# Optimization experiments

Hardware: AMD Instinct MI355X
Metric: run time of the kernel (lower is better)

Reference implementation:

```python
import jax, jax.numpy as jnp
import numpy as np

E = 512
H = 8
D = E // H
HID = 2048
NE = 4
TOPK = 2
EPS = 1e-5
NEG = -1e9


def _ln(x, w, b):
    mu = jnp.mean(x, axis=-1, keepdims=True)
    var = jnp.mean(jnp.square(x - mu), axis=-1, keepdims=True)
    return (x - mu) * jax.lax.rsqrt(var + EPS) * w + b


def _expert(xf, mask, ln1_w, ln1_b, ipw, ipb, opw, opb, ln2_w, ln2_b, w1, b1, w2, b2):
    # xf: [T, E]; mask: [T] bool (allowed keys = routed tokens)
    T = xf.shape[0]
    h = _ln(xf, ln1_w, ln1_b)
    qkv = h @ ipw.T + ipb                       # [T, 3E]
    q, k, v = jnp.split(qkv, 3, axis=-1)
    q = q.reshape(T, H, D).transpose(1, 0, 2)   # [H, T, D]
    k = k.reshape(T, H, D).transpose(1, 0, 2)
    v = v.reshape(T, H, D).transpose(1, 0, 2)
    scores = jnp.einsum('htd,hsd->hts', q, k) / jnp.sqrt(jnp.asarray(D, xf.dtype))
    scores = jnp.where(mask[None, None, :], scores, NEG)
    a = jax.nn.softmax(scores, axis=-1)
    o = jnp.einsum('hts,hsd->htd', a, v).transpose(1, 0, 2).reshape(T, E)
    o = o @ opw.T + opb
    x1 = xf + o                                 # residual (dropout = identity, eval)
    h2 = _ln(x1, ln2_w, ln2_b)
    m = jax.nn.gelu(h2 @ w1.T + b1, approximate=False) @ w2.T + b2
    return x1 + m


def setup_inputs() -> dict:
    key = jax.random.key(0)
    ks = jax.random.split(key, 16)
    s = 0.02
    inp = {
        'x': jax.random.normal(ks[0], (4, 512, E), dtype=jnp.float32),
        'gate_w': jax.random.normal(ks[1], (NE, E), dtype=jnp.float32) * s,
        'gate_b': jnp.zeros((NE,), jnp.float32),
        'ln1_w': jnp.ones((NE, E), jnp.float32),
        'ln1_b': jnp.zeros((NE, E), jnp.float32),
        'in_proj_w': jax.random.normal(ks[2], (NE, 3 * E, E), dtype=jnp.float32) * s,
        'in_proj_b': jnp.zeros((NE, 3 * E), jnp.float32),
        'out_proj_w': jax.random.normal(ks[3], (NE, E, E), dtype=jnp.float32) * s,
        'out_proj_b': jnp.zeros((NE, E), jnp.float32),
        'ln2_w': jnp.ones((NE, E), jnp.float32),
        'ln2_b': jnp.zeros((NE, E), jnp.float32),
        'mlp_w1': jax.random.normal(ks[4], (NE, HID, E), dtype=jnp.float32) * s,
        'mlp_b1': jnp.zeros((NE, HID), jnp.float32),
        'mlp_w2': jax.random.normal(ks[5], (NE, E, HID), dtype=jnp.float32) * s,
        'mlp_b2': jnp.zeros((NE, E), jnp.float32),
    }
    return inp


def reference(x, gate_w, gate_b, ln1_w, ln1_b, in_proj_w, in_proj_b, out_proj_w,
              out_proj_b, ln2_w, ln2_b, mlp_w1, mlp_b1, mlp_w2, mlp_b2):
    B, N, _ = x.shape
    T = B * N
    xf = x.reshape(T, E)
    logits = xf @ gate_w.T + gate_b                      # [T, NE]
    topk_val, topk_idx = jax.lax.top_k(logits, TOPK)
    probs = jax.nn.softmax(topk_val, axis=-1)            # [T, TOPK]
    out = jnp.zeros_like(xf)
    for kk in range(TOPK):
        idx = topk_idx[:, kk]
        w = probs[:, kk][:, None]
        for e in range(NE):
            mask = idx == e
            eo = _expert(xf, mask,
                         ln1_w[e], ln1_b[e], in_proj_w[e], in_proj_b[e],
                         out_proj_w[e], out_proj_b[e], ln2_w[e], ln2_b[e],
                         mlp_w1[e], mlp_b1[e], mlp_w2[e], mlp_b2[e])
            out = out + jnp.where(mask[:, None], eo * w, 0.0)
    return out.reshape(B, N, E)
```

## Files before the change

### kernel.cpp

```cpp
#include <hip/hip_runtime.h>
#include <hip/hip_bf16.h>

#define T_TOK 2048
#define E_DIM 512
#define NHEAD 8
#define DHEAD 64
#define HID_D 2048
#define NEXP 4
#define NROW_ (2 * T_TOK)
#define VT_STRIDE 4352

typedef short short8 __attribute__((ext_vector_type(8)));
typedef float floatx4 __attribute__((ext_vector_type(4)));

__device__ __forceinline__ void gld16(const void* g, void* l) {
  __builtin_amdgcn_global_load_lds((const __attribute__((address_space(1))) void*)g,
                                   (__attribute__((address_space(3))) void*)l, 16, 0, 0);
}

__device__ inline float wave_sum(float v) {
  for (int off = 32; off > 0; off >>= 1) v += __shfl_xor(v, off);
  return v;
}

__device__ __forceinline__ unsigned pack_bf2(float a, float b) {
  __hip_bfloat16 ha = __float2bfloat16(a), hb = __float2bfloat16(b);
  unsigned ua = *(unsigned short*)&ha, ub = *(unsigned short*)&hb;
  return ua | (ub << 16);
}

__device__ __forceinline__ void cvt4(const float* __restrict__ s, __hip_bfloat16* __restrict__ d,
                                     int i4, int n) {
  if (i4 < n) {
    float4 v = *reinterpret_cast<const float4*>(s + i4);
    __hip_bfloat16 tmp[4] = {__float2bfloat16(v.x), __float2bfloat16(v.y),
                             __float2bfloat16(v.z), __float2bfloat16(v.w)};
    *reinterpret_cast<ushort4*>(d + i4) = *reinterpret_cast<const ushort4*>(tmp);
  }
}

__global__ void cvt_weights(const float* __restrict__ s0, const float* __restrict__ s1,
                            const float* __restrict__ s2, const float* __restrict__ s3,
                            __hip_bfloat16* d0, __hip_bfloat16* d1,
                            __hip_bfloat16* d2, __hip_bfloat16* d3,
                            int n0, int n1, int n2, int n3) {
  int i4 = (blockIdx.x * 256 + threadIdx.x) * 4;
  cvt4(s0, d0, i4, n0);
  cvt4(s1, d1, i4, n1);
  cvt4(s2, d2, i4, n2);
  cvt4(s3, d3, i4, n3);
}

__global__ void gate_kernel(const float* __restrict__ x, const float* __restrict__ gw,
                            const float* __restrict__ gb, int* token_e, float* token_p) {
  int wid = threadIdx.x >> 6, lane = threadIdx.x & 63;
  int t = blockIdx.x * 4 + wid;
  float a0 = 0, a1 = 0, a2 = 0, a3 = 0;
  for (int i = 0; i < 8; i++) {
    int c = lane + 64 * i;
    float xv = x[(size_t)t * E_DIM + c];
    a0 += xv * gw[0 * E_DIM + c];
    a1 += xv * gw[1 * E_DIM + c];
    a2 += xv * gw[2 * E_DIM + c];
    a3 += xv * gw[3 * E_DIM + c];
  }
  a0 = wave_sum(a0); a1 = wave_sum(a1); a2 = wave_sum(a2); a3 = wave_sum(a3);
  if (lane == 0) {
    float lg[4] = {a0 + gb[0], a1 + gb[1], a2 + gb[2], a3 + gb[3]};
    int i0 = 0;
    for (int e = 1; e < 4; e++) if (lg[e] > lg[i0]) i0 = e;
    int i1 = -1;
    for (int e = 0; e < 4; e++) {
      if (e == i0) continue;
      if (i1 < 0 || lg[e] > lg[i1]) i1 = e;
    }
    float e1 = __expf(lg[i1] - lg[i0]);
    float inv = 1.f / (1.f + e1);
    token_e[t] = i0; token_e[T_TOK + t] = i1;
    token_p[t] = inv; token_p[T_TOK + t] = e1 * inv;
  }
}

__global__ void count_kernel(const int* __restrict__ token_e, int* counts) {
  int g = blockIdx.x, kk = g >> 2, e = g & 3;
  __shared__ int ws4[4];
  int tid = threadIdx.x, wid = tid >> 6, lane = tid & 63;
  int c = 0;
  for (int t = tid; t < T_TOK; t += 256) c += (token_e[kk * T_TOK + t] == e);
  for (int off = 32; off; off >>= 1) c += __shfl_xor(c, off);
  if (lane == 0) ws4[wid] = c;
  __syncthreads();
  if (tid == 0) counts[g] = ws4[0] + ws4[1] + ws4[2] + ws4[3];
}

__global__ void offs_kernel(const int* __restrict__ counts, int* offs, int* padoffs) {
  int o = 0, po = 0;
  offs[0] = 0; padoffs[0] = 0;
  for (int g = 0; g < 8; g++) {
    o += counts[g]; offs[g + 1] = o;
    po += (counts[g] + 31) & ~31; padoffs[g + 1] = po;
  }
}

__global__ void compact_kernel(const int* __restrict__ token_e, const int* __restrict__ offs,
                               const int* __restrict__ padoffs, int* perm, int* rowg,
                               int* pmap, int* invrow) {
  int g = blockIdx.x, kk = g >> 2, e = g & 3;
  __shared__ int wcnt[4];
  __shared__ int base;
  int tid = threadIdx.x, wid = tid >> 6, lane = tid & 63;
  int og = offs[g], pg = padoffs[g];
  if (tid == 0) base = 0;
  __syncthreads();
  for (int t0 = 0; t0 < T_TOK; t0 += 256) {
    int t = t0 + tid;
    bool pred = token_e[kk * T_TOK + t] == e;
    unsigned long long mask = __ballot(pred);
    int rank = __popcll(mask & ((1ull << lane) - 1ull));
    if (lane == 0) wcnt[wid] = __popcll(mask);
    __syncthreads();
    int woff = 0;
    for (int i = 0; i < wid; i++) woff += wcnt[i];
    if (pred) {
      int row = og + base + woff + rank;
      perm[row] = t;
      rowg[row] = g;
      pmap[row] = pg + (row - og);
      invrow[kk * T_TOK + t] = row;
    }
    __syncthreads();
    if (tid == 0) base += wcnt[0] + wcnt[1] + wcnt[2] + wcnt[3];
    __syncthreads();
  }
}

__global__ void ln_kernel(const float* __restrict__ src, const int* __restrict__ perm,
                          const int* __restrict__ rowg, const float* __restrict__ lnw,
                          const float* __restrict__ lnb, __hip_bfloat16* __restrict__ dst) {
  int wid = threadIdx.x >> 6, lane = threadIdx.x & 63;
  int row = blockIdx.x * 4 + wid;
  int e = rowg[row] & 3;
  const float* xr = src + (size_t)(perm ? perm[row] : row) * E_DIM;
  float v[8];
  float s = 0;
  for (int i = 0; i < 8; i++) { v[i] = xr[lane + 64 * i]; s += v[i]; }
  s = wave_sum(s);
  float mu = s * (1.f / 512.f);
  float q = 0;
  for (int i = 0; i < 8; i++) { float d = v[i] - mu; q += d * d; }
  q = wave_sum(q);
  float rstd = rsqrtf(q * (1.f / 512.f) + 1e-5f);
  for (int i = 0; i < 8; i++) {
    int c = lane + 64 * i;
    dst[(size_t)row * E_DIM + c] =
        __float2bfloat16((v[i] - mu) * rstd * lnw[e * E_DIM + c] + lnb[e * E_DIM + c]);
  }
}

__global__ void transpose_v(const short* __restrict__ v, const int* __restrict__ pmap,
                            short* __restrict__ vT) {
  __shared__ short tile[64][65];
  int r0 = blockIdx.x * 64, c0 = blockIdx.y * 64;
  int tc = threadIdx.x & 63, tr4 = threadIdx.x >> 6;
  for (int i = 0; i < 64; i += 4)
    tile[tr4 + i][tc] = v[(size_t)(r0 + tr4 + i) * E_DIM + c0 + tc];
  __syncthreads();
  int pcol = pmap[r0 + tc];
  for (int i = 0; i < 64; i += 4)
    vT[(size_t)(c0 + tr4 + i) * VT_STRIDE + pcol] = tile[tc][tr4 + i];
}

__global__ void zero_gaps(const int* __restrict__ offs, const int* __restrict__ padoffs,
                          short* __restrict__ vT) {
  int g = blockIdx.x;
  int cnt = offs[g + 1] - offs[g];
  int gap = (padoffs[g + 1] - padoffs[g]) - cnt;
  if ((int)threadIdx.x < gap) {
    int col = padoffs[g] + cnt + threadIdx.x;
    for (int d = blockIdx.y; d < E_DIM; d += gridDim.y)
      vT[(size_t)d * VT_STRIDE + col] = 0;
  }
}

__global__ __launch_bounds__(256) void attn_mfma(
    const short* __restrict__ qb, const short* __restrict__ kb,
    const short* __restrict__ vT, const int* __restrict__ offs,
    const int* __restrict__ padoffs, __hip_bfloat16* __restrict__ ob) {
  int d0 = blockIdx.x;
  int g = d0 & 7;
  int rem = d0 >> 3;
  int h = rem >> 5;
  int qblk = rem & 31;
  int sbeg = offs[g], rend = offs[g + 1];
  int q0 = sbeg + qblk * 64;
  if (q0 >= rend) return;
  int G = rend - sbeg;
  int pg = padoffs[g];
  int tid = threadIdx.x, wid = tid >> 6, lane = tid & 63;
  int fr = lane & 15, lg = lane >> 4;
  int qw = q0 + wid * 16;

  __shared__ short Kt[2][32 * 64];
  __shared__ short Vt[2][64 * 32];

  int arow = qw + fr; if (arow > rend - 1) arow = rend - 1;
  const short* qp = qb + (size_t)arow * E_DIM + h * DHEAD;
  short8 qf0 = *reinterpret_cast<const short8*>(qp + lg * 8);
  short8 qf1 = *reinterpret_cast<const short8*>(qp + 32 + lg * 8);

  int offB = tid * 16;
  int krow = offB >> 7, kinner = offB & 127;
  int ksrc = (kinner ^ ((krow & 7) << 4)) >> 1;
  int vd = offB >> 6, vinner = offB & 63;
  int vsrc = (vinner ^ ((vd & 3) << 4)) >> 1;
  int wb = wid * 512;
  const short* vrow = vT + (size_t)(h * DHEAD + vd) * VT_STRIDE + pg;

  auto stage = [&](int buf, int kbase) {
    int gr = sbeg + kbase + krow; if (gr > NROW_ - 1) gr = NROW_ - 1;
    gld16(kb + (size_t)gr * E_DIM + h * DHEAD + ksrc, &Kt[buf][wb]);
    gld16(vrow + kbase + vsrc, &Vt[buf][wb]);
  };

  floatx4 acc[4] = {};
  float m_r = -1e30f, l_r = 0.f;

  stage(0, 0);
  asm volatile("s_waitcnt vmcnt(0)" ::: "memory");
  __syncthreads();

  int cur = 0;
  for (int kbase = 0; kbase < G; kbase += 32) {
    if (kbase + 32 < G) stage(cur ^ 1, kbase + 32);
    const char* Kb = (const char*)&Kt[cur][0];
    const char* Vb = (const char*)&Vt[cur][0];

    int r0r = fr, r1r = 16 + fr;
    short8 kf00 = *reinterpret_cast<const short8*>(Kb + r0r * 128 + ((lg * 16) ^ ((r0r & 7) << 4)));
    short8 kf01 = *reinterpret_cast<const short8*>(Kb + r0r * 128 + ((64 + lg * 16) ^ ((r0r & 7) << 4)));
    short8 kf10 = *reinterpret_cast<const short8*>(Kb + r1r * 128 + ((lg * 16) ^ ((r1r & 7) << 4)));
    short8 kf11 = *reinterpret_cast<const short8*>(Kb + r1r * 128 + ((64 + lg * 16) ^ ((r1r & 7) << 4)));

    floatx4 s0 = {}, s1 = {};
    s0 = __builtin_amdgcn_mfma_f32_16x16x32_bf16(kf00, qf0, s0, 0, 0, 0);
    s0 = __builtin_amdgcn_mfma_f32_16x16x32_bf16(kf01, qf1, s0, 0, 0, 0);
    s1 = __builtin_amdgcn_mfma_f32_16x16x32_bf16(kf10, qf0, s1, 0, 0, 0);
    s1 = __builtin_amdgcn_mfma_f32_16x16x32_bf16(kf11, qf1, s1, 0, 0, 0);

    float sv[8];
    float mloc = -1e30f;
#pragma unroll
    for (int j = 0; j < 4; j++) {
      int k0 = kbase + lg * 4 + j;
      sv[j] = (k0 < G) ? s0[j] * 0.125f : -1e30f;
      sv[4 + j] = (k0 + 16 < G) ? s1[j] * 0.125f : -1e30f;
      mloc = fmaxf(mloc, fmaxf(sv[j], sv[4 + j]));
    }
    mloc = fmaxf(mloc, __shfl_xor(mloc, 16));
    mloc = fmaxf(mloc, __shfl_xor(mloc, 32));
    float mn = fmaxf(m_r, mloc);
    float corr = __expf(m_r - mn);
    m_r = mn;
    float p[8], sl = 0.f;
#pragma unroll
    for (int i = 0; i < 8; i++) { p[i] = __expf(sv[i] - mn); sl += p[i]; }
    sl += __shfl_xor(sl, 16);
    sl += __shfl_xor(sl, 32);
    l_r = l_r * corr + sl;

    unsigned pk0 = pack_bf2(p[0], p[1]), pk1 = pack_bf2(p[2], p[3]);
    unsigned pk2 = pack_bf2(p[4], p[5]), pk3 = pack_bf2(p[6], p[7]);
    int sA = fr + 16 * (2 * (lg & 1));
    int sB = sA + 16;
    unsigned a0 = __shfl(pk0, sA), a2 = __shfl(pk2, sA);
    unsigned b0 = __shfl(pk1, sA), b2 = __shfl(pk3, sA);
    unsigned c0 = __shfl(pk0, sB), c2 = __shfl(pk2, sB);
    unsigned d0v = __shfl(pk1, sB), d2 = __shfl(pk3, sB);
    bool hi = lg >= 2;
    union { unsigned u[4]; short8 s8; } pfu;
    pfu.u[0] = hi ? a2 : a0; pfu.u[1] = hi ? b2 : b0;
    pfu.u[2] = hi ? c2 : c0; pfu.u[3] = hi ? d2 : d0v;

    float cq[4];
#pragma unroll
    for (int j = 0; j < 4; j++) cq[j] = __shfl(corr, lg * 4 + j);
#pragma unroll
    for (int db = 0; db < 4; db++)
#pragma unroll
      for (int j = 0; j < 4; j++) acc[db][j] *= cq[j];

#pragma unroll
    for (int db = 0; db < 4; db++) {
      int dd = db * 16 + fr;
      short8 vf = *reinterpret_cast<const short8*>(Vb + dd * 64 + ((lg * 16) ^ ((dd & 3) << 4)));
      acc[db] = __builtin_amdgcn_mfma_f32_16x16x32_bf16(pfu.s8, vf, acc[db], 0, 0, 0);
    }

    asm volatile("s_waitcnt vmcnt(0)" ::: "memory");
    __syncthreads();
    cur ^= 1;
  }

  float lq[4];
#pragma unroll
  for (int j = 0; j < 4; j++) lq[j] = __shfl(l_r, lg * 4 + j);
#pragma unroll
  for (int db = 0; db < 4; db++)
#pragma unroll
    for (int j = 0; j < 4; j++) {
      int row = qw + lg * 4 + j;
      if (row < rend)
        ob[(size_t)row * E_DIM + h * DHEAD + db * 16 + fr] = __float2bfloat16(acc[db][j] / lq[j]);
    }
}

template <int MODE>
__global__ __launch_bounds__(256) void gemm_mfma(
    const short* __restrict__ A, const short* __restrict__ Wb,
    const float* __restrict__ bias, const int* __restrict__ offs,
    const int* __restrict__ perm, const float* __restrict__ resid,
    __hip_bfloat16* __restrict__ bq, __hip_bfloat16* __restrict__ bk,
    __hip_bfloat16* __restrict__ bv, float* __restrict__ outf) {
  constexpr int K = (MODE == 3) ? HID_D : E_DIM;
  constexpr int N = (MODE == 0) ? 3 * E_DIM : (MODE == 2) ? HID_D : E_DIM;
  constexpr int NKSTEP = K / 64;
  constexpr int NXB = 32;
  __shared__ short Abuf[2][4096];
  __shared__ short Bbuf[2][4096];

  int d = blockIdx.x;
  int g = d & 7;
  int rem = d >> 3;
  int yb = rem / NXB, xb = rem % NXB;
  int e = g & 3;
  int rbeg = offs[g], rend = offs[g + 1];
  int row0 = rbeg + xb * 64;
  if (row0 >= rend) return;
  int col0 = yb * 64;
  int tid = threadIdx.x;
  int wid = tid >> 6, lane = tid & 63;
  int wm = wid >> 1, wn = wid & 1;
  int fr = lane & 15, lg = lane >> 4;
  const short* wbase = Wb + (size_t)e * N * K;

  int st_row[2], st_src[2], st_arow[2];
  int wavebase = wid << 9;
  for (int c = 0; c < 2; c++) {
    int off = c * 4096 + tid * 16;
    int trow = off >> 7;
    int inner = off & 127;
    st_row[c] = trow;
    st_src[c] = (inner ^ ((trow & 7) << 4)) >> 1;
    int ga = row0 + trow;
    st_arow[c] = ga < rend ? ga : rend - 1;
  }

  auto stage = [&](int buf, int kb) {
#pragma unroll
    for (int c = 0; c < 2; c++) {
      gld16(A + (size_t)st_arow[c] * K + kb + st_src[c], &Abuf[buf][c * 2048 + wavebase]);
      gld16(wbase + (size_t)(col0 + st_row[c]) * K + kb + st_src[c],
            &Bbuf[buf][c * 2048 + wavebase]);
    }
  };

  floatx4 acc[2][2] = {};
  stage(0, 0);
  asm volatile("s_waitcnt vmcnt(0)" ::: "memory");
  __syncthreads();

  int cur = 0;
  for (int t = 0; t < NKSTEP; ++t) {
    if (t + 1 < NKSTEP) stage(cur ^ 1, (t + 1) * 64);
    const char* Ab = (const char*)&Abuf[cur][0];
    const char* Bb = (const char*)&Bbuf[cur][0];
    short8 af[2][2], bf8[2][2];
#pragma unroll
    for (int mi = 0; mi < 2; mi++)
#pragma unroll
      for (int ks = 0; ks < 2; ks++) {
        int row = wm * 32 + mi * 16 + fr;
        int cb = ks * 64 + lg * 16;
        af[mi][ks] = *reinterpret_cast<const short8*>(Ab + row * 128 + (cb ^ ((row & 7) << 4)));
      }
#pragma unroll
    for (int ni = 0; ni < 2; ni++)
#pragma unroll
      for (int ks = 0; ks < 2; ks++) {
        int row = wn * 32 + ni * 16 + fr;
        int cb = ks * 64 + lg * 16;
        bf8[ni][ks] = *reinterpret_cast<const short8*>(Bb + row * 128 + (cb ^ ((row & 7) << 4)));
      }
#pragma unroll
    for (int mi = 0; mi < 2; mi++)
#pragma unroll
      for (int ni = 0; ni < 2; ni++) {
        acc[mi][ni] = __builtin_amdgcn_mfma_f32_16x16x32_bf16(af[mi][0], bf8[ni][0], acc[mi][ni], 0, 0, 0);
        acc[mi][ni] = __builtin_amdgcn_mfma_f32_16x16x32_bf16(af[mi][1], bf8[ni][1], acc[mi][ni], 0, 0, 0);
      }
    asm volatile("s_waitcnt vmcnt(0)" ::: "memory");
    __syncthreads();
    cur ^= 1;
  }

  for (int mi = 0; mi < 2; mi++)
    for (int ni = 0; ni < 2; ni++)
      for (int j = 0; j < 4; j++) {
        int row = row0 + wm * 32 + mi * 16 + lg * 4 + j;
        if (row >= rend) continue;
        int col = col0 + wn * 32 + ni * 16 + fr;
        float val = acc[mi][ni][j] + bias[e * N + col];
        if constexpr (MODE == 0) {
          if (col < E_DIM) bq[(size_t)row * E_DIM + col] = __float2bfloat16(val);
          else if (col < 2 * E_DIM) bk[(size_t)row * E_DIM + col - E_DIM] = __float2bfloat16(val);
          else bv[(size_t)row * E_DIM + col - 2 * E_DIM] = __float2bfloat16(val);
        } else if constexpr (MODE == 1) {
          int t = perm[row];
          outf[(size_t)row * E_DIM + col] = val + resid[(size_t)t * E_DIM + col];
        } else if constexpr (MODE == 2) {
          float gl = 0.5f * val * (1.f + erff(val * 0.70710678118654752f));
          bq[(size_t)row * HID_D + col] = __float2bfloat16(gl);
        } else {
          outf[(size_t)row * E_DIM + col] = val + resid[(size_t)row * E_DIM + col];
        }
      }
}

__global__ void combine_kernel(const float* __restrict__ y, const int* __restrict__ invrow,
                               const float* __restrict__ token_p, float* __restrict__ out) {
  int t = blockIdx.x;
  int r0 = invrow[t], r1 = invrow[T_TOK + t];
  float p0 = token_p[t], p1 = token_p[T_TOK + t];
  const float* y0 = y + (size_t)r0 * E_DIM;
  const float* y1 = y + (size_t)r1 * E_DIM;
  float* o = out + (size_t)t * E_DIM;
  for (int i = threadIdx.x; i < E_DIM; i += 256) o[i] = p0 * y0[i] + p1 * y1[i];
}

extern "C" void kernel_launch(void* const* d_in, const int* in_sizes, int n_in,
                              void* d_out, int out_size, void* d_ws, size_t ws_size,
                              hipStream_t stream) {
  const float* x      = (const float*)d_in[0];
  const float* gate_w = (const float*)d_in[1];
  const float* gate_b = (const float*)d_in[2];
  const float* ln1_w  = (const float*)d_in[3];
  const float* ln1_b  = (const float*)d_in[4];
  const float* ipw    = (const float*)d_in[5];
  const float* ipb    = (const float*)d_in[6];
  const float* opw    = (const float*)d_in[7];
  const float* opb    = (const float*)d_in[8];
  const float* ln2_w  = (const float*)d_in[9];
  const float* ln2_b  = (const float*)d_in[10];
  const float* w1     = (const float*)d_in[11];
  const float* b1     = (const float*)d_in[12];
  const float* w2     = (const float*)d_in[13];
  const float* b2     = (const float*)d_in[14];
  float* out = (float*)d_out;

  const int SZ_IP = NEXP * 3 * E_DIM * E_DIM;
  const int SZ_OP = NEXP * E_DIM * E_DIM;
  const int SZ_W1 = NEXP * HID_D * E_DIM;
  const int SZ_W2 = NEXP * E_DIM * HID_D;
  const int NROW = NROW_;

  char* ws = (char*)d_ws;
  size_t off = 0;
  auto carve = [&](size_t bytes) -> void* {
    void* p = ws + off;
    off += (bytes + 255) & ~(size_t)255;
    return p;
  };
  __hip_bfloat16* ipw_bf = (__hip_bfloat16*)carve((size_t)SZ_IP * 2);
  __hip_bfloat16* opw_bf = (__hip_bfloat16*)carve((size_t)SZ_OP * 2);
  __hip_bfloat16* w1_bf  = (__hip_bfloat16*)carve((size_t)SZ_W1 * 2);
  __hip_bfloat16* w2_bf  = (__hip_bfloat16*)carve((size_t)SZ_W2 * 2);
  __hip_bfloat16* h_bf   = (__hip_bfloat16*)carve((size_t)NROW * E_DIM * 2);
  __hip_bfloat16* q_bf   = (__hip_bfloat16*)carve((size_t)NROW * E_DIM * 2);
  __hip_bfloat16* k_bf   = (__hip_bfloat16*)carve((size_t)NROW * E_DIM * 2);
  __hip_bfloat16* v_bf   = (__hip_bfloat16*)carve((size_t)NROW * E_DIM * 2);
  __hip_bfloat16* o_bf   = (__hip_bfloat16*)carve((size_t)NROW * E_DIM * 2);
  __hip_bfloat16* h2_bf  = (__hip_bfloat16*)carve((size_t)NROW * E_DIM * 2);
  __hip_bfloat16* mid_bf = (__hip_bfloat16*)carve((size_t)NROW * HID_D * 2);
  short* vT     = (short*)carve((size_t)E_DIM * VT_STRIDE * 2);
  float* x1     = (float*)carve((size_t)NROW * E_DIM * 4);
  int* token_e  = (int*)carve((size_t)NROW * 4);
  float* token_p= (float*)carve((size_t)NROW * 4);
  int* perm     = (int*)carve((size_t)NROW * 4);
  int* rowg     = (int*)carve((size_t)NROW * 4);
  int* pmap     = (int*)carve((size_t)NROW * 4);
  int* invrow   = (int*)carve((size_t)NROW * 4);
  int* counts   = (int*)carve(8 * 4);
  int* offs     = (int*)carve(9 * 4);
  int* padoffs  = (int*)carve(9 * 4);
  float* ybuf = (float*)h_bf;

  cvt_weights<<<SZ_W1 / 4 / 256, 256, 0, stream>>>(ipw, opw, w1, w2, ipw_bf, opw_bf,
                                                   w1_bf, w2_bf, SZ_IP, SZ_OP, SZ_W1, SZ_W2);
  gate_kernel<<<T_TOK / 4, 256, 0, stream>>>(x, gate_w, gate_b, token_e, token_p);
  count_kernel<<<8, 256, 0, stream>>>(token_e, counts);
  offs_kernel<<<1, 1, 0, stream>>>(counts, offs, padoffs);
  compact_kernel<<<8, 256, 0, stream>>>(token_e, offs, padoffs, perm, rowg, pmap, invrow);
  ln_kernel<<<NROW / 4, 256, 0, stream>>>(x, perm, rowg, ln1_w, ln1_b, h_bf);
  gemm_mfma<0><<<8 * 24 * 32, 256, 0, stream>>>((const short*)h_bf, (const short*)ipw_bf,
      ipb, offs, perm, nullptr, q_bf, k_bf, v_bf, nullptr);
  transpose_v<<<dim3(NROW / 64, E_DIM / 64), 256, 0, stream>>>((const short*)v_bf, pmap, vT);
  zero_gaps<<<dim3(8, 64), 32, 0, stream>>>(offs, padoffs, vT);
  attn_mfma<<<8 * 8 * 32, 256, 0, stream>>>((const short*)q_bf, (const short*)k_bf,
      vT, offs, padoffs, o_bf);
  gemm_mfma<1><<<8 * 8 * 32, 256, 0, stream>>>((const short*)o_bf, (const short*)opw_bf,
      opb, offs, perm, x, nullptr, nullptr, nullptr, x1);
  ln_kernel<<<NROW / 4, 256, 0, stream>>>(x1, nullptr, rowg, ln2_w, ln2_b, h2_bf);
  gemm_mfma<2><<<8 * 32 * 32, 256, 0, stream>>>((const short*)h2_bf, (const short*)w1_bf,
      b1, offs, perm, nullptr, mid_bf, nullptr, nullptr, nullptr);
  gemm_mfma<3><<<8 * 8 * 32, 256, 0, stream>>>((const short*)mid_bf, (const short*)w2_bf,
      b2, offs, perm, x1, nullptr, nullptr, nullptr, ybuf);
  combine_kernel<<<T_TOK, 256, 0, stream>>>(ybuf, invrow, token_p, out);
  (void)in_sizes; (void)n_in; (void)ws_size;
}
```

Baseline: 194.0 us.

## Skip softmax rescale below threshold and drop P shuffles in attention PV

In the attention kernel, the online-softmax correction (exp, shuffles and rescaling of the accumulators) now runs only when some lane's running max rises by more than a threshold. This is the lazy-rescale trick: it is exact in the end because the normalizer is rescaled consistently, but it relies on the unscaled exponentials staying bounded. The P-to-A-operand cross-lane shuffles are removed. Instead, the kernel issues two half-zeroed MFMAs per output block that read V with a new LDS swizzle matching the score layout, which doubles the PV MFMA count in exchange for fewer shuffles.

```diff
diff --git a/kernel.cpp b/kernel.cpp
--- a/kernel.cpp
+++ b/kernel.cpp
@@ -211,15 +211,15 @@
   int offB = tid * 16;
   int krow = offB >> 7, kinner = offB & 127;
   int ksrc = (kinner ^ ((krow & 7) << 4)) >> 1;
-  int vd = offB >> 6, vinner = offB & 63;
-  int vsrc = (vinner ^ ((vd & 3) << 4)) >> 1;
+  int vL = offB ^ (((offB >> 7) & 7) << 4);
+  int vd = vL >> 6, vkey0 = (vL & 63) >> 1;
   int wb = wid * 512;
   const short* vrow = vT + (size_t)(h * DHEAD + vd) * VT_STRIDE + pg;
 
   auto stage = [&](int buf, int kbase) {
     int gr = sbeg + kbase + krow; if (gr > NROW_ - 1) gr = NROW_ - 1;
     gld16(kb + (size_t)gr * E_DIM + h * DHEAD + ksrc, &Kt[buf][wb]);
-    gld16(vrow + kbase + vsrc, &Vt[buf][wb]);
+    gld16(vrow + kbase + vkey0, &Vt[buf][wb]);
   };
 
   floatx4 acc[4] = {};
@@ -258,42 +258,42 @@
     }
     mloc = fmaxf(mloc, __shfl_xor(mloc, 16));
     mloc = fmaxf(mloc, __shfl_xor(mloc, 32));
-    float mn = fmaxf(m_r, mloc);
-    float corr = __expf(m_r - mn);
-    m_r = mn;
+    if (__any(mloc > m_r + 8.f)) {
+      float mn = fmaxf(m_r, mloc);
+      float corr = __expf(m_r - mn);
+      m_r = mn;
+      l_r *= corr;
+      float cq0 = __shfl(corr, lg * 4 + 0), cq1 = __shfl(corr, lg * 4 + 1);
+      float cq2 = __shfl(corr, lg * 4 + 2), cq3 = __shfl(corr, lg * 4 + 3);
+#pragma unroll
+      for (int db = 0; db < 4; db++) {
+        acc[db][0] *= cq0; acc[db][1] *= cq1; acc[db][2] *= cq2; acc[db][3] *= cq3;
+      }
+    }
     float p[8], sl = 0.f;
 #pragma unroll
-    for (int i = 0; i < 8; i++) { p[i] = __expf(sv[i] - mn); sl += p[i]; }
+    for (int i = 0; i < 8; i++) { p[i] = __expf(sv[i] - m_r); sl += p[i]; }
     sl += __shfl_xor(sl, 16);
     sl += __shfl_xor(sl, 32);
-    l_r = l_r * corr + sl;
-
-    unsigned pk0 = pack_bf2(p[0], p[1]), pk1 = pack_bf2(p[2], p[3]);
-    unsigned pk2 = pack_bf2(p[4], p[5]), pk3 = pack_bf2(p[6], p[7]);
-    int sA = fr + 16 * (2 * (lg & 1));
-    int sB = sA + 16;
-    unsigned a0 = __shfl(pk0, sA), a2 = __shfl(pk2, sA);
-    unsigned b0 = __shfl(pk1, sA), b2 = __shfl(pk3, sA);
-    unsigned c0 = __shfl(pk0, sB), c2 = __shfl(pk2, sB);
-    unsigned d0v = __shfl(pk1, sB), d2 = __shfl(pk3, sB);
-    bool hi = lg >= 2;
-    union { unsigned u[4]; short8 s8; } pfu;
-    pfu.u[0] = hi ? a2 : a0; pfu.u[1] = hi ? b2 : b0;
-    pfu.u[2] = hi ? c2 : c0; pfu.u[3] = hi ? d2 : d0v;
-
-    float cq[4];
-#pragma unroll
-    for (int j = 0; j < 4; j++) cq[j] = __shfl(corr, lg * 4 + j);
-#pragma unroll
-    for (int db = 0; db < 4; db++)
-#pragma unroll
-      for (int j = 0; j < 4; j++) acc[db][j] *= cq[j];
+    l_r += sl;
+
+    union { unsigned u[4]; short8 s8; } pa0, pa1;
+    pa0.u[0] = pack_bf2(p[0], p[1]); pa0.u[1] = pack_bf2(p[2], p[3]);
+    pa0.u[2] = 0; pa0.u[3] = 0;
+    pa1.u[0] = pack_bf2(p[4], p[5]); pa1.u[1] = pack_bf2(p[6], p[7]);
+    pa1.u[2] = 0; pa1.u[3] = 0;
 
 #pragma unroll
     for (int db = 0; db < 4; db++) {
       int dd = db * 16 + fr;
-      short8 vf = *reinterpret_cast<const short8*>(Vb + dd * 64 + ((lg * 16) ^ ((dd & 3) << 4)));
-      acc[db] = __builtin_amdgcn_mfma_f32_16x16x32_bf16(pfu.s8, vf, acc[db], 0, 0, 0);
+      int s = ((dd >> 1) & 7) << 4;
+      uint2 w0 = *reinterpret_cast<const uint2*>(Vb + ((dd * 64 + lg * 8) ^ s));
+      uint2 w1 = *reinterpret_cast<const uint2*>(Vb + ((dd * 64 + 32 + lg * 8) ^ s));
+      union { unsigned u[4]; short8 s8; } bv0, bv1;
+      bv0.u[0] = w0.x; bv0.u[1] = w0.y; bv0.u[2] = 0; bv0.u[3] = 0;
+      bv1.u[0] = w1.x; bv1.u[1] = w1.y; bv1.u[2] = 0; bv1.u[3] = 0;
+      acc[db] = __builtin_amdgcn_mfma_f32_16x16x32_bf16(pa0.s8, bv0.s8, acc[db], 0, 0, 0);
+      acc[db] = __builtin_amdgcn_mfma_f32_16x16x32_bf16(pa1.s8, bv1.s8, acc[db], 0, 0, 0);
     }
 
     asm volatile("s_waitcnt vmcnt(0)" ::: "memory");
@@ -301,9 +301,9 @@
     cur ^= 1;
   }
 
-  float lq[4];
-#pragma unroll
-  for (int j = 0; j < 4; j++) lq[j] = __shfl(l_r, lg * 4 + j);
+  float lq0 = __shfl(l_r, lg * 4 + 0), lq1 = __shfl(l_r, lg * 4 + 1);
+  float lq2 = __shfl(l_r, lg * 4 + 2), lq3 = __shfl(l_r, lg * 4 + 3);
+  float lq[4] = {lq0, lq1, lq2, lq3};
 #pragma unroll
   for (int db = 0; db < 4; db++)
 #pragma unroll
```

Result: faster. 189.8 us (-2.2%).
